# Optimization experiments

Measured on AMD Instinct MI355X. Metric: run time of the kernel, lower is better.

## Reference

```python
import jax, jax.numpy as jnp
import numpy as np

B, N, D, H = 2, 1536, 1024, 16
DH = D // H
SCALE = DH ** -0.5


def setup_inputs() -> dict:
    key = jax.random.key(0)
    ks = jax.random.split(key, 16)
    s = D ** -0.5
    x = jax.random.normal(ks[0], (B, N, D), dtype=jnp.float32)
    # causal prior: 0 on/below diagonal, -1e9 above
    causal = jnp.tril(jnp.ones((N, N), dtype=bool))
    attn_bias = jnp.where(causal, 0.0, -1e9).astype(jnp.float32)[None, None]
    mk = lambda k, shp: jax.random.normal(k, shp, dtype=jnp.float32) * s
    return {
        "x": x,
        "attn_bias": attn_bias,
        "Wq": mk(ks[1], (D, D)), "bq": jnp.zeros((D,), jnp.float32),
        "Wk": mk(ks[2], (D, D)), "bk": jnp.zeros((D,), jnp.float32),
        "Wv": mk(ks[3], (D, D)), "bv": jnp.zeros((D,), jnp.float32),
        "Wg1": mk(ks[4], (D, D)), "bg1": jnp.zeros((D,), jnp.float32),
        "Wg2": mk(ks[5], (D, 1)), "bg2": jnp.zeros((1,), jnp.float32),
        "Wo": mk(ks[6], (D, D)), "bo": jnp.zeros((D,), jnp.float32),
    }


def reference(x, attn_bias, Wq, bq, Wk, bk, Wv, bv, Wg1, bg1, Wg2, bg2, Wo, bo):
    b, n, d = x.shape
    # projections -> [B, H, N, DH]
    split = lambda t: t.reshape(b, n, H, DH).swapaxes(1, 2)
    Q = split(x @ Wq + bq)
    K = split(x @ Wk + bk)
    V = split(x @ Wv + bv)
    # scores [B, H, N, N]
    attn = jnp.einsum("bhnd,bhmd->bhnm", Q, K) * SCALE + attn_bias
    attn = jax.nn.softmax(attn, axis=-1)
    # per-(batch, head, query) entropy over key axis
    entropy = -(attn * jnp.log(attn + 1e-6)).sum(-1)  # [B, H, N]
    # gate MLP (torch nn.GELU default is exact erf)
    gate = jax.nn.sigmoid(jax.nn.gelu(x @ Wg1 + bg1, approximate=False) @ Wg2 + bg2)  # [B, N, 1]
    attn = attn * gate[:, None, :, :]  # broadcast over heads, keys
    out = jnp.einsum("bhnm,bhmd->bhnd", attn, V)
    out = out.swapaxes(1, 2).reshape(b, n, d) @ Wo + bo
    return out, entropy
```

## Files before the change

### kernel.cpp

```cpp
#include <hip/hip_runtime.h>
#include <hip/hip_bf16.h>
#include <math.h>

#define Bsz  2
#define Nseq 1536
#define Dmod 1024
#define NH   16
#define DHd  64
#define MTOT (Bsz*Nseq)
#define SCALE 0.125f
#define BK   32

typedef short  short8 __attribute__((ext_vector_type(8)));
typedef float  f32x4  __attribute__((ext_vector_type(4)));
typedef unsigned short u16x4 __attribute__((ext_vector_type(4)));
typedef unsigned short ushortT;

__device__ __forceinline__ float b2f(__hip_bfloat16 v) { return __bfloat162float(v); }
__device__ __forceinline__ unsigned short f2bf(float f) {
    union { float f; unsigned u; } a; a.f = f;
    unsigned r = a.u + 0x7fffu + ((a.u >> 16) & 1u);
    return (unsigned short)(r >> 16);
}

__device__ __forceinline__ void gl2lds16(const ushortT* g, ushortT* lds) {
    __builtin_amdgcn_global_load_lds(
        (const __attribute__((address_space(1))) unsigned int*)(g),
        (__attribute__((address_space(3))) unsigned int*)(lds),
        16, 0, 0);
}

__global__ __launch_bounds__(256)
void prep_kernel(const float* W0, const float* W1, const float* W2,
                 const float* W3, const float* W4,
                 ushortT* T0, ushortT* T1, ushortT* T2, ushortT* T3, ushortT* T4,
                 const float* __restrict__ x, ushortT* __restrict__ xb,
                 float* __restrict__ glogit)
{
    const int z = blockIdx.z;
    const int t = threadIdx.x;
    if (z == 5) {
        const int bi = blockIdx.y * 16 + blockIdx.x;
        const size_t NEl = (size_t)MTOT * Dmod;
        for (size_t i = ((size_t)bi * 256 + t) * 4; i < NEl; i += (size_t)256 * 256 * 4) {
            float4 v = *(const float4*)(x + i);
            u16x4 o = { f2bf(v.x), f2bf(v.y), f2bf(v.z), f2bf(v.w) };
            *(u16x4*)(xb + i) = o;
        }
        if (t < 12) glogit[bi * 12 + t] = 0.f;
        return;
    }
    __shared__ float tile[64][65];
    const float* W = z == 0 ? W0 : z == 1 ? W1 : z == 2 ? W2 : z == 3 ? W3 : W4;
    ushortT*     T = z == 0 ? T0 : z == 1 ? T1 : z == 2 ? T2 : z == 3 ? T3 : T4;
    const int k0 = blockIdx.x * 64, n0 = blockIdx.y * 64;
    for (int i = t; i < 4096; i += 256) {
        int r = i >> 6, c = i & 63;
        tile[r][c] = W[(size_t)(k0 + r) * 1024 + n0 + c];
    }
    __syncthreads();
    for (int i = t; i < 4096; i += 256) {
        int rn = i >> 6, ck = i & 63;
        T[(size_t)(n0 + rn) * 1024 + k0 + ck] = f2bf(tile[ck][rn]);
    }
}

__device__ __forceinline__
void gemm_core(const ushortT* __restrict__ A, const ushortT* __restrict__ Bt,
               int m0, int n0, ushortT* As, ushortT* Bs, f32x4 (&acc)[4][2])
{
    const int t = threadIdx.x;
    const int l = t & 63, w = t >> 6;
    const int wm = (w >> 1) * 64, wn = (w & 1) * 32;
    const int lm = l & 15, q = l >> 4;

    const int r0 = t >> 2, c0 = (t & 3) * 8;
    const ushortT* Ag0 = A  + (size_t)(m0 + r0) * 1024 + c0;
    const ushortT* Ag1 = Ag0 + (size_t)64 * 1024;
    const ushortT* Bg0 = Bt + (size_t)(n0 + r0) * 1024 + c0;
    ushortT* La0 = As + t * 8;
    ushortT* La1 = As + 2048 + t * 8;
    ushortT* Lb0 = Bs + t * 8;

    gl2lds16(Ag0, La0);
    gl2lds16(Ag1, La1);
    gl2lds16(Bg0, Lb0);

    for (int kt = 0; kt < 1024 / BK; ++kt) {
        __syncthreads();
        if (kt + 1 < 1024 / BK) {
            int ko = (kt + 1) * BK;
            int bo = ((kt + 1) & 1) ? 4096 : 0;
            int bo2 = ((kt + 1) & 1) ? 2048 : 0;
            gl2lds16(Ag0 + ko, La0 + bo);
            gl2lds16(Ag1 + ko, La1 + bo);
            gl2lds16(Bg0 + ko, Lb0 + bo2);
        }
        const ushortT* Ab = As + ((kt & 1) ? 4096 : 0);
        const ushortT* Bb = Bs + ((kt & 1) ? 2048 : 0);
        short8 af[4], bf[2];
#pragma unroll
        for (int i = 0; i < 4; ++i)
            af[i] = *(const short8*)&Ab[(wm + i * 16 + lm) * 32 + q * 8];
#pragma unroll
        for (int j = 0; j < 2; ++j)
            bf[j] = *(const short8*)&Bb[(wn + j * 16 + lm) * 32 + q * 8];
#pragma unroll
        for (int i = 0; i < 4; ++i)
#pragma unroll
            for (int j = 0; j < 2; ++j)
                acc[i][j] = __builtin_amdgcn_mfma_f32_16x16x32_bf16(af[i], bf[j], acc[i][j], 0, 0, 0);
    }
}

__global__ __launch_bounds__(256)
void gemm_qkvg(const ushortT* __restrict__ xb,
               const ushortT* Wt0, const ushortT* Wt1, const ushortT* Wt2, const ushortT* Wt3,
               const float* bz0, const float* bz1, const float* bz2, const float* bz3,
               const float* __restrict__ Wg2,
               ushortT* O0, ushortT* O1, ushortT* O2, float* __restrict__ glogit)
{
    __shared__ ushortT As[2 * 128 * 32];
    __shared__ ushortT Bs[2 * 64 * 32];
    const int z = blockIdx.z;
    const ushortT* Wt  = z == 0 ? Wt0 : z == 1 ? Wt1 : z == 2 ? Wt2 : Wt3;
    const float*  bias = z == 0 ? bz0 : z == 1 ? bz1 : z == 2 ? bz2 : bz3;
    const int m0 = blockIdx.y * 128, n0 = blockIdx.x * 64;

    f32x4 acc[4][2] = {};
    gemm_core(xb, Wt, m0, n0, As, Bs, acc);

    const int t = threadIdx.x, l = t & 63, w = t >> 6;
    const int wm = (w >> 1) * 64, wn = (w & 1) * 32;
    const int lm = l & 15, q = l >> 4;

    if (z == 3) {
        float part[4][4] = {};
#pragma unroll
        for (int i = 0; i < 4; ++i)
#pragma unroll
            for (int j = 0; j < 2; ++j) {
                int n = n0 + wn + j * 16 + lm;
                float bn = bias[n];
                float w2 = Wg2[n];
#pragma unroll
                for (int r = 0; r < 4; ++r) {
                    float v = acc[i][j][r] + bn;
                    v = 0.5f * v * (1.0f + erff(v * 0.70710678118654752f));
                    part[i][r] += v * w2;
                }
            }
#pragma unroll
        for (int i = 0; i < 4; ++i)
#pragma unroll
            for (int r = 0; r < 4; ++r) {
                float p = part[i][r];
#pragma unroll
                for (int msk = 1; msk < 16; msk <<= 1) p += __shfl_xor(p, msk, 16);
                if (lm == 0)
                    atomicAdd(&glogit[m0 + wm + i * 16 + q * 4 + r], p);
            }
        return;
    }

    ushortT* O = z == 0 ? O0 : z == 1 ? O1 : O2;
#pragma unroll
    for (int i = 0; i < 4; ++i)
#pragma unroll
        for (int j = 0; j < 2; ++j) {
            int n = n0 + wn + j * 16 + lm;
            float bn = bias[n];
#pragma unroll
            for (int r = 0; r < 4; ++r) {
                int m = m0 + wm + i * 16 + q * 4 + r;
                float v = acc[i][j][r] + bn;
                if (z == 0) v *= SCALE;
                if (z == 2) {
                    int b = m / Nseq, nn = m - b * Nseq;
                    int h = n >> 6, dd = n & 63;
                    O[(size_t)((b * 16 + h) * 64 + dd) * Nseq + nn] = f2bf(v);
                } else {
                    O[(size_t)m * 1024 + n] = f2bf(v);
                }
            }
        }
}

__global__ __launch_bounds__(256)
void gemm_out(const ushortT* __restrict__ AO, const ushortT* __restrict__ WtO,
              const float* __restrict__ bias, float* __restrict__ C)
{
    __shared__ ushortT As[2 * 128 * 32];
    __shared__ ushortT Bs[2 * 64 * 32];
    const int m0 = blockIdx.y * 128, n0 = blockIdx.x * 64;

    f32x4 acc[4][2] = {};
    gemm_core(AO, WtO, m0, n0, As, Bs, acc);

    const int t = threadIdx.x, l = t & 63, w = t >> 6;
    const int wm = (w >> 1) * 64, wn = (w & 1) * 32;
    const int lm = l & 15, q = l >> 4;
#pragma unroll
    for (int i = 0; i < 4; ++i)
#pragma unroll
        for (int j = 0; j < 2; ++j) {
            int n = n0 + wn + j * 16 + lm;
            float bn = bias[n];
#pragma unroll
            for (int r = 0; r < 4; ++r) {
                int m = m0 + wm + i * 16 + q * 4 + r;
                C[(size_t)m * 1024 + n] = acc[i][j][r] + bn;
            }
        }
}

__global__ __launch_bounds__(64)
void attn_mfma(const ushortT* __restrict__ Q, const ushortT* __restrict__ K,
               const ushortT* __restrict__ Vt, const float* __restrict__ glogit,
               const float* __restrict__ bg2, ushortT* __restrict__ AO,
               float* __restrict__ ent)
{
    __shared__ ushortT Ps[32][72];

    const int l  = threadIdx.x;
    const int ln = l & 15, q4 = l >> 4;
    const int bh = blockIdx.x, b = bh >> 4, h = bh & 15;
    const int q32 = (int)gridDim.y - 1 - (int)blockIdx.y;
    const int wq = q32 * 32;
    const int kd = wq >> 6;
    const int sbmax = ((wq >> 4) & 3) + 1;

    const ushortT* Qp = Q + (size_t)(b * Nseq + wq + ln) * Dmod + h * DHd + q4 * 8;
    short8 qf[2][2];
    qf[0][0] = *(const short8*)(Qp);
    qf[0][1] = *(const short8*)(Qp + 32);
    qf[1][0] = *(const short8*)(Qp + (size_t)16 * Dmod);
    qf[1][1] = *(const short8*)(Qp + (size_t)16 * Dmod + 32);

    float l_lane[2][4] = {}, t_lane[2][4] = {};
    f32x4 oacc[2][4] = {};

    const ushortT* Kbase = K  + (size_t)(b * Nseq) * Dmod + h * DHd + q4 * 8;
    const ushortT* Vbase = Vt + ((size_t)(b * 16 + h) * 64) * Nseq + q4 * 8;

    short8 kc[4][2];
    {
        const ushortT* Kp = Kbase + (size_t)ln * Dmod;
#pragma unroll
        for (int nb = 0; nb < 4; ++nb) {
            kc[nb][0] = *(const short8*)(Kp + (size_t)nb * 16 * Dmod);
            kc[nb][1] = *(const short8*)(Kp + (size_t)nb * 16 * Dmod + 32);
        }
    }

    for (int kt = 0; kt < kd; ++kt) {
        const int k0 = kt * 64;
        const ushortT* Vp = Vbase + (size_t)ln * Nseq + k0;
        short8 vf[4][2];
#pragma unroll
        for (int nb = 0; nb < 4; ++nb) {
            vf[nb][0] = *(const short8*)(Vp + (size_t)nb * 16 * Nseq);
            vf[nb][1] = *(const short8*)(Vp + (size_t)nb * 16 * Nseq + 32);
        }
        short8 kn[4][2];
        {
            const ushortT* Kp = Kbase + (size_t)(k0 + 64 + ln) * Dmod;
#pragma unroll
            for (int nb = 0; nb < 4; ++nb) {
                kn[nb][0] = *(const short8*)(Kp + (size_t)nb * 16 * Dmod);
                kn[nb][1] = *(const short8*)(Kp + (size_t)nb * 16 * Dmod + 32);
            }
        }
        f32x4 sacc[2][4];
#pragma unroll
        for (int g = 0; g < 2; ++g)
#pragma unroll
            for (int nb = 0; nb < 4; ++nb) {
                f32x4 a = {};
                a = __builtin_amdgcn_mfma_f32_16x16x32_bf16(qf[g][0], kc[nb][0], a, 0, 0, 0);
                a = __builtin_amdgcn_mfma_f32_16x16x32_bf16(qf[g][1], kc[nb][1], a, 0, 0, 0);
                sacc[g][nb] = a;
            }
#pragma unroll
        for (int g = 0; g < 2; ++g)
#pragma unroll
            for (int nb = 0; nb < 4; ++nb)
#pragma unroll
                for (int r = 0; r < 4; ++r) {
                    float sv = sacc[g][nb][r];
                    float ev = __expf(sv);
                    l_lane[g][r] += ev;
                    t_lane[g][r] += ev * sv;
                    Ps[g * 16 + q4 * 4 + r][nb * 16 + ln] = f2bf(ev);
                }
        short8 pf[2][2];
#pragma unroll
        for (int g = 0; g < 2; ++g) {
            pf[g][0] = *(const short8*)&Ps[g * 16 + ln][q4 * 8];
            pf[g][1] = *(const short8*)&Ps[g * 16 + ln][32 + q4 * 8];
        }
#pragma unroll
        for (int g = 0; g < 2; ++g)
#pragma unroll
            for (int nb = 0; nb < 4; ++nb) {
                oacc[g][nb] = __builtin_amdgcn_mfma_f32_16x16x32_bf16(pf[g][0], vf[nb][0], oacc[g][nb], 0, 0, 0);
                oacc[g][nb] = __builtin_amdgcn_mfma_f32_16x16x32_bf16(pf[g][1], vf[nb][1], oacc[g][nb], 0, 0, 0);
            }
#pragma unroll
        for (int nb = 0; nb < 4; ++nb) { kc[nb][0] = kn[nb][0]; kc[nb][1] = kn[nb][1]; }
    }

    {
        const int k0 = kd * 64;
        const ushortT* Vp = Vbase + (size_t)ln * Nseq + k0;
        short8 vf[4][2];
#pragma unroll
        for (int nb = 0; nb < 4; ++nb) {
            vf[nb][0] = *(const short8*)(Vp + (size_t)nb * 16 * Nseq);
            vf[nb][1] = *(const short8*)(Vp + (size_t)nb * 16 * Nseq + 32);
        }
        f32x4 sacc[2][4];
#pragma unroll
        for (int g = 0; g < 2; ++g)
#pragma unroll
            for (int nb = 0; nb < 4; ++nb)
                if (nb <= sbmax) {
                    f32x4 a = {};
                    a = __builtin_amdgcn_mfma_f32_16x16x32_bf16(qf[g][0], kc[nb][0], a, 0, 0, 0);
                    a = __builtin_amdgcn_mfma_f32_16x16x32_bf16(qf[g][1], kc[nb][1], a, 0, 0, 0);
                    sacc[g][nb] = a;
                }
#pragma unroll
        for (int g = 0; g < 2; ++g)
#pragma unroll
            for (int nb = 0; nb < 4; ++nb)
#pragma unroll
                for (int r = 0; r < 4; ++r) {
                    float ev = 0.f;
                    if (nb <= sbmax) {
                        int kg = k0 + nb * 16 + ln;
                        int qg = wq + g * 16 + q4 * 4 + r;
                        float sv = sacc[g][nb][r];
                        ev = (kg <= qg) ? __expf(sv) : 0.f;
                        l_lane[g][r] += ev;
                        t_lane[g][r] += ev * sv;
                    }
                    Ps[g * 16 + q4 * 4 + r][nb * 16 + ln] = f2bf(ev);
                }
        short8 pf[2][2];
#pragma unroll
        for (int g = 0; g < 2; ++g) {
            pf[g][0] = *(const short8*)&Ps[g * 16 + ln][q4 * 8];
            pf[g][1] = *(const short8*)&Ps[g * 16 + ln][32 + q4 * 8];
        }
#pragma unroll
        for (int g = 0; g < 2; ++g)
#pragma unroll
            for (int nb = 0; nb < 4; ++nb) {
                oacc[g][nb] = __builtin_amdgcn_mfma_f32_16x16x32_bf16(pf[g][0], vf[nb][0], oacc[g][nb], 0, 0, 0);
                oacc[g][nb] = __builtin_amdgcn_mfma_f32_16x16x32_bf16(pf[g][1], vf[nb][1], oacc[g][nb], 0, 0, 0);
            }
    }

    const float bg2v = bg2[0];
#pragma unroll
    for (int g = 0; g < 2; ++g) {
        float sc[4];
#pragma unroll
        for (int r = 0; r < 4; ++r) {
            float lv = l_lane[g][r], tv = t_lane[g][r];
#pragma unroll
            for (int msk = 1; msk < 16; msk <<= 1) {
                lv += __shfl_xor(lv, msk, 16);
                tv += __shfl_xor(tv, msk, 16);
            }
            int qg = wq + g * 16 + q4 * 4 + r;
            float inv = 1.f / lv;
            if (ln == 0)
                ent[((size_t)b * NH + h) * Nseq + qg] = logf(lv) - tv * inv;
            float logit = glogit[b * Nseq + qg] + bg2v;
            sc[r] = inv / (1.f + __expf(-logit));
        }
#pragma unroll
        for (int nb = 0; nb < 4; ++nb)
#pragma unroll
            for (int r = 0; r < 4; ++r) {
                int qg = wq + g * 16 + q4 * 4 + r;
                AO[(size_t)(b * Nseq + qg) * Dmod + h * DHd + nb * 16 + ln] =
                    f2bf(oacc[g][nb][r] * sc[r]);
            }
    }
}

extern "C" void kernel_launch(void* const* d_in, const int* in_sizes, int n_in,
                              void* d_out, int out_size, void* d_ws, size_t ws_size,
                              hipStream_t stream)
{
    const float* x   = (const float*)d_in[0];
    const float* Wq  = (const float*)d_in[2];
    const float* bq  = (const float*)d_in[3];
    const float* Wk  = (const float*)d_in[4];
    const float* bk  = (const float*)d_in[5];
    const float* Wv  = (const float*)d_in[6];
    const float* bv  = (const float*)d_in[7];
    const float* Wg1 = (const float*)d_in[8];
    const float* bg1 = (const float*)d_in[9];
    const float* Wg2 = (const float*)d_in[10];
    const float* bg2 = (const float*)d_in[11];
    const float* Wo  = (const float*)d_in[12];
    const float* bo  = (const float*)d_in[13];

    const size_t NE = (size_t)MTOT * Dmod;
    ushortT* p   = (ushortT*)d_ws;
    ushortT* Qw  = p; p += NE;
    ushortT* Kw  = p; p += NE;
    ushortT* Vtw = p; p += NE;
    ushortT* AO  = p; p += NE;
    ushortT* xb  = p; p += NE;
    ushortT* WtQ = p; p += (size_t)1024 * 1024;
    ushortT* WtK = p; p += (size_t)1024 * 1024;
    ushortT* WtV = p; p += (size_t)1024 * 1024;
    ushortT* WtG = p; p += (size_t)1024 * 1024;
    ushortT* WtO = p; p += (size_t)1024 * 1024;
    float* glogit = (float*)p;

    float* out_f = (float*)d_out;
    float* ent_f = out_f + NE;

    prep_kernel<<<dim3(16, 16, 6), 256, 0, stream>>>(Wq, Wk, Wv, Wg1, Wo,
                                                     WtQ, WtK, WtV, WtG, WtO,
                                                     x, xb, glogit);
    gemm_qkvg<<<dim3(16, 24, 4), 256, 0, stream>>>(xb, WtQ, WtK, WtV, WtG,
                                                   bq, bk, bv, bg1, Wg2,
                                                   Qw, Kw, Vtw, glogit);
    attn_mfma<<<dim3(Bsz * NH, Nseq / 32), 64, 0, stream>>>(Qw, Kw, Vtw, glogit,
                                                            bg2, AO, ent_f);
    gemm_out<<<dim3(16, 24), 256, 0, stream>>>(AO, WtO, bo, out_f);
}
```

Baseline: 234.0 us.

## Split attention key loop across two waves and widen QKVG GEMM tile

The QKV/gate projection GEMM now uses a 128x128 output tile with a 4x4 MFMA accumulator per wave, which halves the grid and raises reuse of each loaded A/B tile. The attention kernel runs two waves per block that take alternating 64-key blocks. Their partial output accumulators and softmax/entropy sums are then merged through shared memory before the epilogue. The aim is to shorten the serial key loop for long causal rows and cut global traffic in the GEMM, at the cost of more registers and LDS per block and an extra reduction step.

```diff
diff --git a/kernel.cpp b/kernel.cpp
--- a/kernel.cpp
+++ b/kernel.cpp
@@ -66,8 +66,58 @@
 }
 
 __device__ __forceinline__
-void gemm_core(const ushortT* __restrict__ A, const ushortT* __restrict__ Bt,
-               int m0, int n0, ushortT* As, ushortT* Bs, f32x4 (&acc)[4][2])
+void gemm_core128(const ushortT* __restrict__ A, const ushortT* __restrict__ Bt,
+                  int m0, int n0, ushortT* As, ushortT* Bs, f32x4 (&acc)[4][4])
+{
+    const int t = threadIdx.x;
+    const int l = t & 63, w = t >> 6;
+    const int wm = (w >> 1) * 64, wn = (w & 1) * 64;
+    const int lm = l & 15, q = l >> 4;
+
+    const int r0 = t >> 2, c0 = (t & 3) * 8;
+    const ushortT* Ag0 = A  + (size_t)(m0 + r0) * 1024 + c0;
+    const ushortT* Ag1 = Ag0 + (size_t)64 * 1024;
+    const ushortT* Bg0 = Bt + (size_t)(n0 + r0) * 1024 + c0;
+    const ushortT* Bg1 = Bg0 + (size_t)64 * 1024;
+    ushortT* La0 = As + t * 8;
+    ushortT* La1 = As + 2048 + t * 8;
+    ushortT* Lb0 = Bs + t * 8;
+    ushortT* Lb1 = Bs + 2048 + t * 8;
+
+    gl2lds16(Ag0, La0);
+    gl2lds16(Ag1, La1);
+    gl2lds16(Bg0, Lb0);
+    gl2lds16(Bg1, Lb1);
+
+    for (int kt = 0; kt < 1024 / BK; ++kt) {
+        __syncthreads();
+        if (kt + 1 < 1024 / BK) {
+            int ko = (kt + 1) * BK;
+            int bo = ((kt + 1) & 1) ? 4096 : 0;
+            gl2lds16(Ag0 + ko, La0 + bo);
+            gl2lds16(Ag1 + ko, La1 + bo);
+            gl2lds16(Bg0 + ko, Lb0 + bo);
+            gl2lds16(Bg1 + ko, Lb1 + bo);
+        }
+        const ushortT* Ab = As + ((kt & 1) ? 4096 : 0);
+        const ushortT* Bb = Bs + ((kt & 1) ? 4096 : 0);
+        short8 af[4], bf[4];
+#pragma unroll
+        for (int i = 0; i < 4; ++i) {
+            af[i] = *(const short8*)&Ab[(wm + i * 16 + lm) * 32 + q * 8];
+            bf[i] = *(const short8*)&Bb[(wn + i * 16 + lm) * 32 + q * 8];
+        }
+#pragma unroll
+        for (int i = 0; i < 4; ++i)
+#pragma unroll
+            for (int j = 0; j < 4; ++j)
+                acc[i][j] = __builtin_amdgcn_mfma_f32_16x16x32_bf16(af[i], bf[j], acc[i][j], 0, 0, 0);
+    }
+}
+
+__device__ __forceinline__
+void gemm_core64(const ushortT* __restrict__ A, const ushortT* __restrict__ Bt,
+                 int m0, int n0, ushortT* As, ushortT* Bs, f32x4 (&acc)[4][2])
 {
     const int t = threadIdx.x;
     const int l = t & 63, w = t >> 6;
@@ -121,17 +171,17 @@
                ushortT* O0, ushortT* O1, ushortT* O2, float* __restrict__ glogit)
 {
     __shared__ ushortT As[2 * 128 * 32];
-    __shared__ ushortT Bs[2 * 64 * 32];
+    __shared__ ushortT Bs[2 * 128 * 32];
     const int z = blockIdx.z;
     const ushortT* Wt  = z == 0 ? Wt0 : z == 1 ? Wt1 : z == 2 ? Wt2 : Wt3;
     const float*  bias = z == 0 ? bz0 : z == 1 ? bz1 : z == 2 ? bz2 : bz3;
-    const int m0 = blockIdx.y * 128, n0 = blockIdx.x * 64;
-
-    f32x4 acc[4][2] = {};
-    gemm_core(xb, Wt, m0, n0, As, Bs, acc);
+    const int m0 = blockIdx.y * 128, n0 = blockIdx.x * 128;
+
+    f32x4 acc[4][4] = {};
+    gemm_core128(xb, Wt, m0, n0, As, Bs, acc);
 
     const int t = threadIdx.x, l = t & 63, w = t >> 6;
-    const int wm = (w >> 1) * 64, wn = (w & 1) * 32;
+    const int wm = (w >> 1) * 64, wn = (w & 1) * 64;
     const int lm = l & 15, q = l >> 4;
 
     if (z == 3) {
@@ -139,7 +189,7 @@
 #pragma unroll
         for (int i = 0; i < 4; ++i)
 #pragma unroll
-            for (int j = 0; j < 2; ++j) {
+            for (int j = 0; j < 4; ++j) {
                 int n = n0 + wn + j * 16 + lm;
                 float bn = bias[n];
                 float w2 = Wg2[n];
@@ -167,7 +217,7 @@
 #pragma unroll
     for (int i = 0; i < 4; ++i)
 #pragma unroll
-        for (int j = 0; j < 2; ++j) {
+        for (int j = 0; j < 4; ++j) {
             int n = n0 + wn + j * 16 + lm;
             float bn = bias[n];
 #pragma unroll
@@ -195,7 +245,7 @@
     const int m0 = blockIdx.y * 128, n0 = blockIdx.x * 64;
 
     f32x4 acc[4][2] = {};
-    gemm_core(AO, WtO, m0, n0, As, Bs, acc);
+    gemm_core64(AO, WtO, m0, n0, As, Bs, acc);
 
     const int t = threadIdx.x, l = t & 63, w = t >> 6;
     const int wm = (w >> 1) * 64, wn = (w & 1) * 32;
@@ -214,15 +264,17 @@
         }
 }
 
-__global__ __launch_bounds__(64)
+__global__ __launch_bounds__(128)
 void attn_mfma(const ushortT* __restrict__ Q, const ushortT* __restrict__ K,
                const ushortT* __restrict__ Vt, const float* __restrict__ glogit,
                const float* __restrict__ bg2, ushortT* __restrict__ AO,
                float* __restrict__ ent)
 {
-    __shared__ ushortT Ps[32][72];
-
-    const int l  = threadIdx.x;
+    __shared__ ushortT Ps[2][32][72];
+    __shared__ float mbuf[3072];
+
+    const int t  = threadIdx.x;
+    const int w  = t >> 6, l = t & 63;
     const int ln = l & 15, q4 = l >> 4;
     const int bh = blockIdx.x, b = bh >> 4, h = bh & 15;
     const int q32 = (int)gridDim.y - 1 - (int)blockIdx.y;
@@ -245,7 +297,7 @@
 
     short8 kc[4][2];
     {
-        const ushortT* Kp = Kbase + (size_t)ln * Dmod;
+        const ushortT* Kp = Kbase + (size_t)(w * 64 + ln) * Dmod;
 #pragma unroll
         for (int nb = 0; nb < 4; ++nb) {
             kc[nb][0] = *(const short8*)(Kp + (size_t)nb * 16 * Dmod);
@@ -253,7 +305,7 @@
         }
     }
 
-    for (int kt = 0; kt < kd; ++kt) {
+    for (int kt = w; kt < kd; kt += 2) {
         const int k0 = kt * 64;
         const ushortT* Vp = Vbase + (size_t)ln * Nseq + k0;
         short8 vf[4][2];
@@ -264,7 +316,8 @@
         }
         short8 kn[4][2];
         {
-            const ushortT* Kp = Kbase + (size_t)(k0 + 64 + ln) * Dmod;
+            int prow = k0 + 128; if (prow > Nseq - 64) prow = Nseq - 64;
+            const ushortT* Kp = Kbase + (size_t)(prow + ln) * Dmod;
 #pragma unroll
             for (int nb = 0; nb < 4; ++nb) {
                 kn[nb][0] = *(const short8*)(Kp + (size_t)nb * 16 * Dmod);
@@ -291,13 +344,13 @@
                     float ev = __expf(sv);
                     l_lane[g][r] += ev;
                     t_lane[g][r] += ev * sv;
-                    Ps[g * 16 + q4 * 4 + r][nb * 16 + ln] = f2bf(ev);
+                    Ps[w][g * 16 + q4 * 4 + r][nb * 16 + ln] = f2bf(ev);
                 }
         short8 pf[2][2];
 #pragma unroll
         for (int g = 0; g < 2; ++g) {
-            pf[g][0] = *(const short8*)&Ps[g * 16 + ln][q4 * 8];
-            pf[g][1] = *(const short8*)&Ps[g * 16 + ln][32 + q4 * 8];
+            pf[g][0] = *(const short8*)&Ps[w][g * 16 + ln][q4 * 8];
+            pf[g][1] = *(const short8*)&Ps[w][g * 16 + ln][32 + q4 * 8];
         }
 #pragma unroll
         for (int g = 0; g < 2; ++g)
@@ -310,7 +363,7 @@
         for (int nb = 0; nb < 4; ++nb) { kc[nb][0] = kn[nb][0]; kc[nb][1] = kn[nb][1]; }
     }
 
-    {
+    if ((kd & 1) == w) {
         const int k0 = kd * 64;
         const ushortT* Vp = Vbase + (size_t)ln * Nseq + k0;
         short8 vf[4][2];
@@ -345,13 +398,13 @@
                         l_lane[g][r] += ev;
                         t_lane[g][r] += ev * sv;
                     }
-                    Ps[g * 16 + q4 * 4 + r][nb * 16 + ln] = f2bf(ev);
+                    Ps[w][g * 16 + q4 * 4 + r][nb * 16 + ln] = f2bf(ev);
                 }
         short8 pf[2][2];
 #pragma unroll
         for (int g = 0; g < 2; ++g) {
-            pf[g][0] = *(const short8*)&Ps[g * 16 + ln][q4 * 8];
-            pf[g][1] = *(const short8*)&Ps[g * 16 + ln][32 + q4 * 8];
+            pf[g][0] = *(const short8*)&Ps[w][g * 16 + ln][q4 * 8];
+            pf[g][1] = *(const short8*)&Ps[w][g * 16 + ln][32 + q4 * 8];
         }
 #pragma unroll
         for (int g = 0; g < 2; ++g)
@@ -360,6 +413,38 @@
                 oacc[g][nb] = __builtin_amdgcn_mfma_f32_16x16x32_bf16(pf[g][0], vf[nb][0], oacc[g][nb], 0, 0, 0);
                 oacc[g][nb] = __builtin_amdgcn_mfma_f32_16x16x32_bf16(pf[g][1], vf[nb][1], oacc[g][nb], 0, 0, 0);
             }
+    }
+
+    if (w == 1) {
+#pragma unroll
+        for (int g = 0; g < 2; ++g)
+#pragma unroll
+            for (int nb = 0; nb < 4; ++nb)
+#pragma unroll
+                for (int r = 0; r < 4; ++r)
+                    mbuf[(((g << 2) | nb) * 4 + r) * 64 + l] = oacc[g][nb][r];
+#pragma unroll
+        for (int g = 0; g < 2; ++g)
+#pragma unroll
+            for (int r = 0; r < 4; ++r) {
+                mbuf[2048 + ((g << 2) | r) * 64 + l] = l_lane[g][r];
+                mbuf[2560 + ((g << 2) | r) * 64 + l] = t_lane[g][r];
+            }
+    }
+    __syncthreads();
+    if (w == 1) return;
+#pragma unroll
+    for (int g = 0; g < 2; ++g) {
+#pragma unroll
+        for (int nb = 0; nb < 4; ++nb)
+#pragma unroll
+            for (int r = 0; r < 4; ++r)
+                oacc[g][nb][r] += mbuf[(((g << 2) | nb) * 4 + r) * 64 + l];
+#pragma unroll
+        for (int r = 0; r < 4; ++r) {
+            l_lane[g][r] += mbuf[2048 + ((g << 2) | r) * 64 + l];
+            t_lane[g][r] += mbuf[2560 + ((g << 2) | r) * 64 + l];
+        }
     }
 
     const float bg2v = bg2[0];
@@ -430,10 +515,10 @@
     prep_kernel<<<dim3(16, 16, 6), 256, 0, stream>>>(Wq, Wk, Wv, Wg1, Wo,
                                                      WtQ, WtK, WtV, WtG, WtO,
                                                      x, xb, glogit);
-    gemm_qkvg<<<dim3(16, 24, 4), 256, 0, stream>>>(xb, WtQ, WtK, WtV, WtG,
-                                                   bq, bk, bv, bg1, Wg2,
-                                                   Qw, Kw, Vtw, glogit);
-    attn_mfma<<<dim3(Bsz * NH, Nseq / 32), 64, 0, stream>>>(Qw, Kw, Vtw, glogit,
-                                                            bg2, AO, ent_f);
+    gemm_qkvg<<<dim3(8, 24, 4), 256, 0, stream>>>(xb, WtQ, WtK, WtV, WtG,
+                                                  bq, bk, bv, bg1, Wg2,
+                                                  Qw, Kw, Vtw, glogit);
+    attn_mfma<<<dim3(Bsz * NH, Nseq / 32), 128, 0, stream>>>(Qw, Kw, Vtw, glogit,
+                                                             bg2, AO, ent_f);
     gemm_out<<<dim3(16, 24), 256, 0, stream>>>(AO, WtO, bo, out_f);
 }
```

Result: slower. 267.6 us (+14.4%).

## Split attention key loop across two waves and merge partials via LDS

Applied to the files above, without the earlier changes.

The attention kernel now launches two wavefronts per query block. Each wave handles alternating 64-key tiles, and the diagonal tile goes to whichever wave owns it. Wave 1 writes its output accumulators and its softmax-sum and entropy partials to shared memory, and wave 0 adds them in before the epilogue. This halves the serial key-loop length per block to get more parallelism on long causal rows. The cost is extra LDS traffic, a block-wide barrier, and doubled K/V prefetch streams.

```diff
diff --git a/kernel.cpp b/kernel.cpp
--- a/kernel.cpp
+++ b/kernel.cpp
@@ -214,15 +214,17 @@
         }
 }
 
-__global__ __launch_bounds__(64)
+__global__ __launch_bounds__(128)
 void attn_mfma(const ushortT* __restrict__ Q, const ushortT* __restrict__ K,
                const ushortT* __restrict__ Vt, const float* __restrict__ glogit,
                const float* __restrict__ bg2, ushortT* __restrict__ AO,
                float* __restrict__ ent)
 {
-    __shared__ ushortT Ps[32][72];
-
-    const int l  = threadIdx.x;
+    __shared__ ushortT Ps[2][32][72];
+    __shared__ float mbuf[3072];
+
+    const int t  = threadIdx.x;
+    const int w  = t >> 6, l = t & 63;
     const int ln = l & 15, q4 = l >> 4;
     const int bh = blockIdx.x, b = bh >> 4, h = bh & 15;
     const int q32 = (int)gridDim.y - 1 - (int)blockIdx.y;
@@ -245,7 +247,7 @@
 
     short8 kc[4][2];
     {
-        const ushortT* Kp = Kbase + (size_t)ln * Dmod;
+        const ushortT* Kp = Kbase + (size_t)(w * 64 + ln) * Dmod;
 #pragma unroll
         for (int nb = 0; nb < 4; ++nb) {
             kc[nb][0] = *(const short8*)(Kp + (size_t)nb * 16 * Dmod);
@@ -253,7 +255,7 @@
         }
     }
 
-    for (int kt = 0; kt < kd; ++kt) {
+    for (int kt = w; kt < kd; kt += 2) {
         const int k0 = kt * 64;
         const ushortT* Vp = Vbase + (size_t)ln * Nseq + k0;
         short8 vf[4][2];
@@ -264,7 +266,8 @@
         }
         short8 kn[4][2];
         {
-            const ushortT* Kp = Kbase + (size_t)(k0 + 64 + ln) * Dmod;
+            int prow = k0 + 128; if (prow > Nseq - 64) prow = Nseq - 64;
+            const ushortT* Kp = Kbase + (size_t)(prow + ln) * Dmod;
 #pragma unroll
             for (int nb = 0; nb < 4; ++nb) {
                 kn[nb][0] = *(const short8*)(Kp + (size_t)nb * 16 * Dmod);
@@ -291,13 +294,13 @@
                     float ev = __expf(sv);
                     l_lane[g][r] += ev;
                     t_lane[g][r] += ev * sv;
-                    Ps[g * 16 + q4 * 4 + r][nb * 16 + ln] = f2bf(ev);
+                    Ps[w][g * 16 + q4 * 4 + r][nb * 16 + ln] = f2bf(ev);
                 }
         short8 pf[2][2];
 #pragma unroll
         for (int g = 0; g < 2; ++g) {
-            pf[g][0] = *(const short8*)&Ps[g * 16 + ln][q4 * 8];
-            pf[g][1] = *(const short8*)&Ps[g * 16 + ln][32 + q4 * 8];
+            pf[g][0] = *(const short8*)&Ps[w][g * 16 + ln][q4 * 8];
+            pf[g][1] = *(const short8*)&Ps[w][g * 16 + ln][32 + q4 * 8];
         }
 #pragma unroll
         for (int g = 0; g < 2; ++g)
@@ -310,7 +313,7 @@
         for (int nb = 0; nb < 4; ++nb) { kc[nb][0] = kn[nb][0]; kc[nb][1] = kn[nb][1]; }
     }
 
-    {
+    if ((kd & 1) == w) {
         const int k0 = kd * 64;
         const ushortT* Vp = Vbase + (size_t)ln * Nseq + k0;
         short8 vf[4][2];
@@ -345,13 +348,13 @@
                         l_lane[g][r] += ev;
                         t_lane[g][r] += ev * sv;
                     }
-                    Ps[g * 16 + q4 * 4 + r][nb * 16 + ln] = f2bf(ev);
+                    Ps[w][g * 16 + q4 * 4 + r][nb * 16 + ln] = f2bf(ev);
                 }
         short8 pf[2][2];
 #pragma unroll
         for (int g = 0; g < 2; ++g) {
-            pf[g][0] = *(const short8*)&Ps[g * 16 + ln][q4 * 8];
-            pf[g][1] = *(const short8*)&Ps[g * 16 + ln][32 + q4 * 8];
+            pf[g][0] = *(const short8*)&Ps[w][g * 16 + ln][q4 * 8];
+            pf[g][1] = *(const short8*)&Ps[w][g * 16 + ln][32 + q4 * 8];
         }
 #pragma unroll
         for (int g = 0; g < 2; ++g)
@@ -360,6 +363,38 @@
                 oacc[g][nb] = __builtin_amdgcn_mfma_f32_16x16x32_bf16(pf[g][0], vf[nb][0], oacc[g][nb], 0, 0, 0);
                 oacc[g][nb] = __builtin_amdgcn_mfma_f32_16x16x32_bf16(pf[g][1], vf[nb][1], oacc[g][nb], 0, 0, 0);
             }
+    }
+
+    if (w == 1) {
+#pragma unroll
+        for (int g = 0; g < 2; ++g)
+#pragma unroll
+            for (int nb = 0; nb < 4; ++nb)
+#pragma unroll
+                for (int r = 0; r < 4; ++r)
+                    mbuf[(((g << 2) | nb) * 4 + r) * 64 + l] = oacc[g][nb][r];
+#pragma unroll
+        for (int g = 0; g < 2; ++g)
+#pragma unroll
+            for (int r = 0; r < 4; ++r) {
+                mbuf[2048 + ((g << 2) | r) * 64 + l] = l_lane[g][r];
+                mbuf[2560 + ((g << 2) | r) * 64 + l] = t_lane[g][r];
+            }
+    }
+    __syncthreads();
+    if (w == 1) return;
+#pragma unroll
+    for (int g = 0; g < 2; ++g) {
+#pragma unroll
+        for (int nb = 0; nb < 4; ++nb)
+#pragma unroll
+            for (int r = 0; r < 4; ++r)
+                oacc[g][nb][r] += mbuf[(((g << 2) | nb) * 4 + r) * 64 + l];
+#pragma unroll
+        for (int r = 0; r < 4; ++r) {
+            l_lane[g][r] += mbuf[2048 + ((g << 2) | r) * 64 + l];
+            t_lane[g][r] += mbuf[2560 + ((g << 2) | r) * 64 + l];
+        }
     }
 
     const float bg2v = bg2[0];
@@ -433,7 +468,7 @@
     gemm_qkvg<<<dim3(16, 24, 4), 256, 0, stream>>>(xb, WtQ, WtK, WtV, WtG,
                                                    bq, bk, bv, bg1, Wg2,
                                                    Qw, Kw, Vtw, glogit);
-    attn_mfma<<<dim3(Bsz * NH, Nseq / 32), 64, 0, stream>>>(Qw, Kw, Vtw, glogit,
-                                                            bg2, AO, ent_f);
+    attn_mfma<<<dim3(Bsz * NH, Nseq / 32), 128, 0, stream>>>(Qw, Kw, Vtw, glogit,
+                                                             bg2, AO, ent_f);
     gemm_out<<<dim3(16, 24), 256, 0, stream>>>(AO, WtO, bo, out_f);
 }
```

Result: no change. 230.1 us (-1.7%).
